# Kernel optimization log

Measured on AMD Instinct MI355X. Metric: run time of the kernel, lower is better.

## Reference

```python
import jax, jax.numpy as jnp
import numpy as np

P_CLAMP = 10.0      # opt.p
OUTPUT_SCALE = 0.1  # opt.output_scale
S_LR = 0.1          # s_lr passed to step()
R_DIM, C_DIM, HID, NLAYERS = 8192, 2048, 20, 2


def _lstm_one_step(x, h0, c0, layers):
    # x: (B, 1) single-time-step input; h0, c0: (NLAYERS, B, HID)
    # torch gate order: i, f, g, o
    inp = x
    for l, (Wih, Whh, bih, bhh) in enumerate(layers):
        gates = inp @ Wih.T + bih + h0[l] @ Whh.T + bhh  # (B, 4H)
        i, f, g, o = jnp.split(gates, 4, axis=-1)
        c = jax.nn.sigmoid(f) * c0[l] + jax.nn.sigmoid(i) * jnp.tanh(g)
        inp = jax.nn.sigmoid(o) * jnp.tanh(c)
    return inp  # last-layer hidden state (B, HID)


def _orth_proj(M, G):
    # tangent projection on the Stiefel manifold
    A = M.T @ G                      # (c, c)
    A_sym = 0.5 * (A + A.T)
    return G - M @ A_sym


def _retraction(M, P):
    Q, R = jnp.linalg.qr(M + P)      # reduced QR, M+P is (r, c), r >= c
    sign = jnp.sign(jnp.sign(jnp.diagonal(R)) + 0.5)  # maps 0 -> +1
    return Q * sign[None, :]


def _log_sign_diag(gram_diag):
    # diagonal of LogAndSign_Preprocess_Gradient: clamp(log|x|/p, -1, 1)
    return jnp.clip(jnp.log(jnp.abs(gram_diag)) / P_CLAMP, -1.0, 1.0)[:, None]


def reference(s, s_grad, L_h0, L_c0, R_h0, R_c0, L_before, R_before,
              W_ih0, W_hh0, b_ih0, b_hh0, W_ih1, W_hh1, b_ih1, b_hh1,
              L_W, L_b, R_W, R_b):
    s0 = s.shape[0]
    M = s.reshape(s0, -1).T                   # (r, c)
    M_grad = s_grad.reshape(s0, -1).T * S_LR  # (r, c)
    r, c = M.shape
    G = _orth_proj(M, M_grad)
    # only the diagonals of GG^T/c and G^TG/r are ever used by the preprocess
    ggt_diag = jnp.sum(G * G, axis=1) / c     # (r,)
    gtg_diag = jnp.sum(G * G, axis=0) / r     # (c,)
    layers = [(W_ih0, W_hh0, b_ih0, b_hh0), (W_ih1, W_hh1, b_ih1, b_hh1)]
    hl = _lstm_one_step(_log_sign_diag(ggt_diag), L_h0, L_c0, layers)  # (r, H)
    hr = _lstm_one_step(_log_sign_diag(gtg_diag), R_h0, R_c0, layers)  # (c, H)
    l_ = (hl @ L_W.T + L_b).squeeze(-1) * OUTPUT_SCALE
    l_ = l_ - l_.mean() + 1.0
    r_ = (hr @ R_W.T + R_b).squeeze(-1) * OUTPUT_SCALE
    r_ = r_ - r_.mean() + 1.0
    Lv = jnp.maximum(l_, L_before)            # diag matrices stored as vectors
    Rv = jnp.maximum(r_, R_before)
    P = Lv[:, None] * G * Rv[None, :]         # L @ G @ R with diagonal L, R
    P = _orth_proj(M, P)
    new_s = _retraction(M, -P).T.reshape(s.shape)
    return new_s


def setup_inputs() -> dict:
    key = jax.random.key(0)
    ks = jax.random.split(key, 16)
    H4 = 4 * HID
    return {
        "s": jax.random.normal(ks[0], (C_DIM, R_DIM), jnp.float32) * 0.02,
        "s_grad": jax.random.normal(ks[1], (C_DIM, R_DIM), jnp.float32) * 0.02,
        "L_h0": jax.random.normal(ks[2], (NLAYERS, R_DIM, HID), jnp.float32) * 0.1,
        "L_c0": jax.random.normal(ks[3], (NLAYERS, R_DIM, HID), jnp.float32) * 0.1,
        "R_h0": jax.random.normal(ks[4], (NLAYERS, C_DIM, HID), jnp.float32) * 0.1,
        "R_c0": jax.random.normal(ks[5], (NLAYERS, C_DIM, HID), jnp.float32) * 0.1,
        "L_before": jnp.ones((R_DIM,), jnp.float32),
        "R_before": jnp.ones((C_DIM,), jnp.float32),
        "W_ih0": jax.random.normal(ks[6], (H4, 1), jnp.float32) * 0.2,
        "W_hh0": jax.random.normal(ks[7], (H4, HID), jnp.float32) * 0.2,
        "b_ih0": jax.random.normal(ks[8], (H4,), jnp.float32) * 0.1,
        "b_hh0": jax.random.normal(ks[9], (H4,), jnp.float32) * 0.1,
        "W_ih1": jax.random.normal(ks[10], (H4, HID), jnp.float32) * 0.2,
        "W_hh1": jax.random.normal(ks[11], (H4, HID), jnp.float32) * 0.2,
        "b_ih1": jax.random.normal(ks[12], (H4,), jnp.float32) * 0.1,
        "b_hh1": jax.random.normal(ks[13], (H4,), jnp.float32) * 0.1,
        "L_W": jax.random.normal(ks[14], (1, HID), jnp.float32) * 0.2,
        "L_b": jnp.zeros((1,), jnp.float32),
        "R_W": jax.random.normal(ks[15], (1, HID), jnp.float32) * 0.2,
        "R_b": jnp.zeros((1,), jnp.float32),
    }
```

## Files before the change

kernel.cpp:

```cpp
#include <hip/hip_runtime.h>
#include <math.h>

#define RD 8192
#define CD 2048

typedef _Float16 f16x8 __attribute__((ext_vector_type(8)));
typedef _Float16 f16x4 __attribute__((ext_vector_type(4)));
typedef float    f32x4 __attribute__((ext_vector_type(4)));

#define GLOBAL_AS __attribute__((address_space(1)))
#define LDS_AS    __attribute__((address_space(3)))

__global__ __launch_bounds__(256) void gemm_nt_f16(
    const _Float16* __restrict__ A, const _Float16* __restrict__ B,
    float* __restrict__ Cp, _Float16* __restrict__ Of16,
    const float* __restrict__ Dg, const _Float16* __restrict__ Eg,
    int M, int N, int K, int ksplit, float beta, float gamma, float sgn)
{
  __shared__ __align__(1024) _Float16 As[2][128 * 32];
  __shared__ __align__(1024) _Float16 Bs[2][128 * 32];
  const int tid = threadIdx.x;
  const int wave = tid >> 6, lane = tid & 63;
  const int wy = wave >> 1, wx = wave & 1;
  const int bi = blockIdx.y * 128, bj = blockIdx.x * 128;
  const int kchunk = K / ksplit;
  const long k0 = (long)blockIdx.z * kchunk;

  f32x4 acc[4][4];
#pragma unroll
  for (int i = 0; i < 4; ++i)
#pragma unroll
    for (int j = 0; j < 4; ++j) acc[i][j] = (f32x4){0.f, 0.f, 0.f, 0.f};

  const int srow = wave * 16 + (lane >> 2);
  const int skof = (lane & 3) * 8;
  const _Float16* aA = A + (long)(bi + srow) * K + k0 + skof;
  const _Float16* aB = B + (long)(bj + srow) * K + k0 + skof;
  const int ldso = wave * 16 * 32;

#define STAGE(buf, kt)                                                         \
  {                                                                            \
    _Float16* lA = &As[buf][ldso];                                             \
    _Float16* lB = &Bs[buf][ldso];                                             \
    _Pragma("unroll")                                                          \
    for (int q = 0; q < 2; ++q) {                                              \
      __builtin_amdgcn_global_load_lds(                                        \
          (const GLOBAL_AS unsigned int*)(aA + (long)q * 64 * K + (kt)),       \
          (LDS_AS unsigned int*)(lA + q * 64 * 32), 16, 0, 0);                 \
      __builtin_amdgcn_global_load_lds(                                        \
          (const GLOBAL_AS unsigned int*)(aB + (long)q * 64 * K + (kt)),       \
          (LDS_AS unsigned int*)(lB + q * 64 * 32), 16, 0, 0);                 \
    }                                                                          \
  }

  const int fr = lane & 15;
  const int fk = (lane >> 4) * 8;

  STAGE(0, 0);
  __syncthreads();
  int cur = 0;
  for (int kt = 0; kt < kchunk; kt += 32) {
    if (kt + 32 < kchunk) STAGE(cur ^ 1, kt + 32);

    f16x8 af[4], bf[4];
#pragma unroll
    for (int t = 0; t < 4; ++t) {
      af[t] = *(const f16x8*)(&As[cur][(wy * 64 + t * 16 + fr) * 32 + fk]);
      bf[t] = *(const f16x8*)(&Bs[cur][(wx * 64 + t * 16 + fr) * 32 + fk]);
    }
#pragma unroll
    for (int mt = 0; mt < 4; ++mt)
#pragma unroll
      for (int nt = 0; nt < 4; ++nt)
        acc[mt][nt] = __builtin_amdgcn_mfma_f32_16x16x32_f16(af[mt], bf[nt], acc[mt][nt], 0, 0, 0);

    __syncthreads();
    cur ^= 1;
  }
#undef STAGE

  const int quad = lane >> 4, fc = lane & 15;
  if (Cp) {
#pragma unroll
    for (int mt = 0; mt < 4; ++mt)
#pragma unroll
      for (int nt = 0; nt < 4; ++nt) {
        const int col = bj + wx * 64 + nt * 16 + fc;
#pragma unroll
        for (int reg = 0; reg < 4; ++reg) {
          const int row = bi + wy * 64 + mt * 16 + quad * 4 + reg;
          atomicAdd(&Cp[(long)row * N + col], acc[mt][nt][reg]);
        }
      }
  } else {
#pragma unroll
    for (int mt = 0; mt < 4; ++mt)
#pragma unroll
      for (int nt = 0; nt < 4; ++nt) {
        const int col = bj + wx * 64 + nt * 16 + fc;
#pragma unroll
        for (int reg = 0; reg < 4; ++reg) {
          const int row = bi + wy * 64 + mt * 16 + quad * 4 + reg;
          const long off = (long)row * N + col;
          float v = sgn * acc[mt][nt][reg];
          if (Dg) v += beta * Dg[off];
          if (Eg) v += gamma * (float)Eg[off];
          Of16[off] = (_Float16)v;
        }
      }
  }
}

__global__ __launch_bounds__(256) void sym_combine(
    const float* __restrict__ Cp, float* __restrict__ out, int n, int nsplit, float scale)
{
  __shared__ float Ts[64][68];
  const int tid = threadIdx.x;
  const int tx = tid & 15, ty = tid >> 4;
  const int bi = blockIdx.y * 64, bj = blockIdx.x * 64;
  float acc[4][4];
#pragma unroll
  for (int i = 0; i < 4; ++i)
#pragma unroll
    for (int j = 0; j < 4; ++j) acc[i][j] = 0.f;

  for (int s = 0; s < nsplit; ++s) {
    const float* C = Cp + (long)s * n * n;
#pragma unroll
    for (int i = 0; i < 4; ++i) {
      float4 v = *(const float4*)(C + (long)(bi + ty * 4 + i) * n + bj + tx * 4);
      acc[i][0] += v.x; acc[i][1] += v.y; acc[i][2] += v.z; acc[i][3] += v.w;
    }
    __syncthreads();
#pragma unroll
    for (int i = 0; i < 4; ++i) {
      float4 w = *(const float4*)(C + (long)(bj + ty * 4 + i) * n + bi + tx * 4);
      *(float4*)&Ts[ty * 4 + i][tx * 4] = w;
    }
    __syncthreads();
#pragma unroll
    for (int i = 0; i < 4; ++i)
#pragma unroll
      for (int j = 0; j < 4; ++j) acc[i][j] += Ts[tx * 4 + j][ty * 4 + i];
  }
#pragma unroll
  for (int i = 0; i < 4; ++i) {
    float4 v; v.x = scale * acc[i][0]; v.y = scale * acc[i][1]; v.z = scale * acc[i][2]; v.w = scale * acc[i][3];
    *(float4*)(out + (long)(bi + ty * 4 + i) * n + bj + tx * 4) = v;
  }
}

__global__ __launch_bounds__(256) void cast_f16(const float* __restrict__ s, _Float16* __restrict__ d)
{
  const long i = ((long)blockIdx.x * 256 + threadIdx.x) * 4;
  float4 v = *(const float4*)(s + i);
  f16x4 o; o[0] = (_Float16)v.x; o[1] = (_Float16)v.y; o[2] = (_Float16)v.z; o[3] = (_Float16)v.w;
  *(f16x4*)(d + i) = o;
}

__global__ __launch_bounds__(256) void cast_f32(const _Float16* __restrict__ s, float* __restrict__ d)
{
  const long i = ((long)blockIdx.x * 256 + threadIdx.x) * 8;
  f16x8 v = *(const f16x8*)(s + i);
  float4 a, b;
  a.x = (float)v[0]; a.y = (float)v[1]; a.z = (float)v[2]; a.w = (float)v[3];
  b.x = (float)v[4]; b.y = (float)v[5]; b.z = (float)v[6]; b.w = (float)v[7];
  *(float4*)(d + i) = a;
  *(float4*)(d + i + 4) = b;
}

__global__ __launch_bounds__(256) void transpose_cast_f16(
    const float* __restrict__ src, _Float16* __restrict__ dst)
{
  __shared__ float T[64][65];
  const int tid = threadIdx.x, tx = tid & 15, ty = tid >> 4;
  const int r0 = blockIdx.x * 64, c0 = blockIdx.y * 64;
#pragma unroll
  for (int i = 0; i < 4; ++i) {
    float4 v = *(const float4*)(src + (long)(c0 + ty * 4 + i) * RD + r0 + tx * 4);
    T[ty * 4 + i][tx * 4 + 0] = v.x; T[ty * 4 + i][tx * 4 + 1] = v.y;
    T[ty * 4 + i][tx * 4 + 2] = v.z; T[ty * 4 + i][tx * 4 + 3] = v.w;
  }
  __syncthreads();
#pragma unroll
  for (int i = 0; i < 4; ++i) {
    f16x4 o;
#pragma unroll
    for (int j = 0; j < 4; ++j) o[j] = (_Float16)T[tx * 4 + j][ty * 4 + i];
    *(f16x4*)(dst + (long)(r0 + ty * 4 + i) * CD + c0 + tx * 4) = o;
  }
}

__global__ __launch_bounds__(256) void transpose_f16(
    const _Float16* __restrict__ src, _Float16* __restrict__ dst)
{
  __shared__ _Float16 T[64][72];
  const int tid = threadIdx.x;
  const int r0 = blockIdx.y * 64;
  const int c0 = blockIdx.x * 64;
  const int sr = tid >> 2, sc = (tid & 3) * 16;
  {
    f16x8 a = *(const f16x8*)(src + (long)(r0 + sr) * RD + c0 + sc);
    f16x8 b = *(const f16x8*)(src + (long)(r0 + sr) * RD + c0 + sc + 8);
    *(f16x8*)&T[sr][sc] = a;
    *(f16x8*)&T[sr][sc + 8] = b;
  }
  __syncthreads();
  {
    f16x8 a, b;
#pragma unroll
    for (int q = 0; q < 8; ++q) { a[q] = T[sc + q][sr]; b[q] = T[sc + 8 + q][sr]; }
    *(f16x8*)(dst + (long)(c0 + sr) * CD + r0 + sc) = a;
    *(f16x8*)(dst + (long)(c0 + sr) * CD + r0 + sc + 8) = b;
  }
}

__global__ __launch_bounds__(256) void row_sumsq(const _Float16* __restrict__ G, float* __restrict__ out, float inv)
{
  __shared__ float red[256];
  const int tid = threadIdx.x;
  const _Float16* row = G + (long)blockIdx.x * RD;
  float s = 0.f;
  for (int c = tid * 8; c < RD; c += 2048) {
    f16x8 v = *(const f16x8*)(row + c);
#pragma unroll
    for (int u = 0; u < 8; ++u) { float f = (float)v[u]; s += f * f; }
  }
  red[tid] = s; __syncthreads();
  for (int off = 128; off > 0; off >>= 1) { if (tid < off) red[tid] += red[tid + off]; __syncthreads(); }
  if (tid == 0) out[blockIdx.x] = red[0] * inv;
}

__global__ __launch_bounds__(256) void col_sumsq(const _Float16* __restrict__ G, float* __restrict__ out)
{
  const int rr = blockIdx.x * 256 + threadIdx.x;
  const int cc0 = blockIdx.y * 256;
  float s = 0.f;
  for (int i = 0; i < 256; ++i) {
    float v = (float)G[(long)(cc0 + i) * RD + rr];
    s += v * v;
  }
  atomicAdd(&out[rr], s * (1.f / (float)CD));
}

__device__ __forceinline__ float sigm_(float x) { return 1.f / (1.f + __expf(-x)); }
__device__ __forceinline__ float tanh_(float x) { float e = __expf(2.f * x); return 1.f - 2.f / (e + 1.f); }

__global__ __launch_bounds__(256) void lstm_head(
    const float* __restrict__ diag, int B,
    const float* __restrict__ h0, const float* __restrict__ c0,
    const float* __restrict__ Wih0, const float* __restrict__ Whh0,
    const float* __restrict__ bih0, const float* __restrict__ bhh0,
    const float* __restrict__ Wih1, const float* __restrict__ Whh1,
    const float* __restrict__ bih1, const float* __restrict__ bhh1,
    const float* __restrict__ HW, const float* __restrict__ Hb,
    float* __restrict__ pre, float* __restrict__ sum_out)
{
  __shared__ float w0[80], wh0[1600], b0[80], wi1[1600], wh1[1600], b1[80], hw[20];
  __shared__ float red[256];
  const int tid = threadIdx.x;
  for (int i = tid; i < 80; i += 256) { w0[i] = Wih0[i]; b0[i] = bih0[i] + bhh0[i]; b1[i] = bih1[i] + bhh1[i]; }
  for (int i = tid; i < 1600; i += 256) { wh0[i] = Whh0[i]; wi1[i] = Wih1[i]; wh1[i] = Whh1[i]; }
  if (tid < 20) hw[tid] = HW[tid];
  __syncthreads();

  const int b = blockIdx.x * 256 + tid;
  const float d = diag[b];
  float x = logf(fabsf(d)) * 0.1f;
  x = fminf(fmaxf(x, -1.f), 1.f);

  const float* h0p = h0 + (long)b * 20;
  const float* c0p = c0 + (long)b * 20;
  const float* h1p = h0 + (long)B * 20 + (long)b * 20;
  const float* c1p = c0 + (long)B * 20 + (long)b * 20;

  float h0r[20], hA[20];
#pragma unroll
  for (int m = 0; m < 20; ++m) h0r[m] = h0p[m];
#pragma unroll
  for (int h = 0; h < 20; ++h) {
    float gi = w0[h] * x + b0[h];
    float gf = w0[20 + h] * x + b0[20 + h];
    float gg = w0[40 + h] * x + b0[40 + h];
    float go = w0[60 + h] * x + b0[60 + h];
#pragma unroll
    for (int m = 0; m < 20; ++m) {
      const float hm = h0r[m];
      gi += wh0[h * 20 + m] * hm;
      gf += wh0[(20 + h) * 20 + m] * hm;
      gg += wh0[(40 + h) * 20 + m] * hm;
      go += wh0[(60 + h) * 20 + m] * hm;
    }
    const float cc = sigm_(gf) * c0p[h] + sigm_(gi) * tanh_(gg);
    hA[h] = sigm_(go) * tanh_(cc);
  }
  float h1r[20];
#pragma unroll
  for (int m = 0; m < 20; ++m) h1r[m] = h1p[m];
  float pr = 0.f;
#pragma unroll
  for (int h = 0; h < 20; ++h) {
    float gi = b1[h], gf = b1[20 + h], gg = b1[40 + h], go = b1[60 + h];
#pragma unroll
    for (int m = 0; m < 20; ++m) {
      const float am = hA[m], hm = h1r[m];
      gi += wi1[h * 20 + m] * am + wh1[h * 20 + m] * hm;
      gf += wi1[(20 + h) * 20 + m] * am + wh1[(20 + h) * 20 + m] * hm;
      gg += wi1[(40 + h) * 20 + m] * am + wh1[(40 + h) * 20 + m] * hm;
      go += wi1[(60 + h) * 20 + m] * am + wh1[(60 + h) * 20 + m] * hm;
    }
    const float cc = sigm_(gf) * c1p[h] + sigm_(gi) * tanh_(gg);
    pr += sigm_(go) * tanh_(cc) * hw[h];
  }
  pr = (pr + Hb[0]) * 0.1f;
  pre[b] = pr;

  red[tid] = pr; __syncthreads();
  for (int off = 128; off > 0; off >>= 1) { if (tid < off) red[tid] += red[tid + off]; __syncthreads(); }
  if (tid == 0) atomicAdd(sum_out, red[0]);
}

__global__ __launch_bounds__(256) void scale_P(
    _Float16* __restrict__ G, const float* __restrict__ lpre, const float* __restrict__ rpre,
    const float* __restrict__ Lbef, const float* __restrict__ Rbef, const float* __restrict__ sums)
{
  const long id4 = ((long)blockIdx.x * 256 + threadIdx.x) * 4;
  const int cc = (int)(id4 >> 13);
  const int rr = (int)(id4 & (RD - 1));
  const float meanl = sums[0] * (1.f / (float)RD);
  const float meanr = sums[1] * (1.f / (float)CD);
  const float rv = fmaxf(rpre[cc] - meanr + 1.f, Rbef[cc]);
  f16x4 g = *(f16x4*)(G + id4);
  float4 lp = *(const float4*)(lpre + rr);
  float4 lb = *(const float4*)(Lbef + rr);
  g[0] = (_Float16)((float)g[0] * rv * fmaxf(lp.x - meanl + 1.f, lb.x));
  g[1] = (_Float16)((float)g[1] * rv * fmaxf(lp.y - meanl + 1.f, lb.y));
  g[2] = (_Float16)((float)g[2] * rv * fmaxf(lp.z - meanl + 1.f, lb.z));
  g[3] = (_Float16)((float)g[3] * rv * fmaxf(lp.w - meanl + 1.f, lb.w));
  *(f16x4*)(G + id4) = g;
}

__device__ __forceinline__ void potrf_block_dev(
    float* __restrict__ S, float* __restrict__ W, float* __restrict__ KinvA,
    int d, int kprev, float (*Ls)[68], float (*Ws)[68], float (*Ts)[68])
{
  const int tid = threadIdx.x;
  const int tx = tid & 15, ty = tid >> 4;
  const long dofs = (long)d * 64;

  for (int t = tid; t < 4096; t += 256) {
    int r = t >> 6, c = t & 63;
    Ls[r][c] = S[(dofs + r) * CD + dofs + c];
  }

  if (kprev >= 0) {
    const float* Kp = KinvA + (long)kprev * 4096;
    const long ko = (long)kprev * 64;
    for (int t = tid; t < 4096; t += 256) {
      int r = t >> 6, c = t & 63;
      Ts[r][c] = S[(dofs + r) * CD + ko + c];
      Ws[r][c] = Kp[t];
    }
    __syncthreads();
    float u[4][4];
#pragma unroll
    for (int i = 0; i < 4; ++i)
#pragma unroll
      for (int j = 0; j < 4; ++j) u[i][j] = 0.f;
    for (int m = 0; m < 64; ++m) {
      float a[4], k2[4];
#pragma unroll
      for (int q = 0; q < 4; ++q) { a[q] = Ts[ty * 4 + q][m]; k2[q] = Ws[m][tx * 4 + q]; }
#pragma unroll
      for (int i = 0; i < 4; ++i)
#pragma unroll
        for (int j = 0; j < 4; ++j) u[i][j] += a[i] * k2[j];
    }
    __syncthreads();
#pragma unroll
    for (int i = 0; i < 4; ++i)
#pragma unroll
      for (int j = 0; j < 4; ++j) Ws[ty * 4 + i][tx * 4 + j] = u[i][j];
    __syncthreads();
    float acc[4][4];
#pragma unroll
    for (int i = 0; i < 4; ++i)
#pragma unroll
      for (int j = 0; j < 4; ++j) acc[i][j] = 0.f;
    for (int m = 0; m < 64; ++m) {
      float a[4], b2[4];
#pragma unroll
      for (int q = 0; q < 4; ++q) { a[q] = Ws[ty * 4 + q][m]; b2[q] = Ts[tx * 4 + q][m]; }
#pragma unroll
      for (int i = 0; i < 4; ++i)
#pragma unroll
        for (int j = 0; j < 4; ++j) acc[i][j] += a[i] * b2[j];
    }
#pragma unroll
    for (int i = 0; i < 4; ++i)
#pragma unroll
      for (int j = 0; j < 4; ++j) Ls[ty * 4 + i][tx * 4 + j] -= acc[i][j];
  }

  for (int j = 0; j < 64; ++j) {
    __syncthreads();
    const float invd = 1.f / Ls[j][j];
    for (int i = j + 1 + ty; i < 64; i += 16) {
      const float vi = Ls[i][j] * invd;
      for (int c = j + 1 + tx; c <= i; c += 16)
        Ls[i][c] -= vi * Ls[c][j];
    }
  }
  __syncthreads();
  if (tid < 64) Ts[0][tid] = 1.f / sqrtf(Ls[tid][tid]);
  __syncthreads();
  for (int t = tid; t < 4096; t += 256) {
    int r = t >> 6, c = t & 63;
    if (c <= r) Ls[r][c] *= Ts[0][c];
  }
  for (int t = tid; t < 4096; t += 256) { int r = t >> 6, c = t & 63; Ws[r][c] = 0.f; }
  __syncthreads();

  {
    const int w = tid >> 6, l = tid & 63;
    if (l < 16) {
      const int o = w * 16, c = l;
      float wr[16];
#pragma unroll
      for (int m = 0; m < 16; ++m) {
        float s = 0.f;
#pragma unroll
        for (int k = 0; k < m; ++k) s += Ls[o + m][o + k] * wr[k];
        const float rli = 1.f / Ls[o + m][o + m];
        wr[m] = (m == c) ? rli : -s * rli;
      }
#pragma unroll
      for (int m = 0; m < 16; ++m) Ws[o + m][o + c] = (m < c) ? 0.f : wr[m];
    }
  }
  __syncthreads();

  {
    for (int e = tid; e < 512; e += 256) {
      const int p = e >> 8, m = (e >> 4) & 15, c = e & 15, b0 = p * 32;
      float s = 0.f;
#pragma unroll
      for (int k = 0; k < 16; ++k) s += Ls[b0 + 16 + m][b0 + k] * Ws[b0 + k][b0 + c];
      Ts[p * 16 + m][c] = s;
    }
    __syncthreads();
    for (int e = tid; e < 512; e += 256) {
      const int p = e >> 8, m = (e >> 4) & 15, c = e & 15, b0 = p * 32;
      float s = 0.f;
#pragma unroll
      for (int k = 0; k < 16; ++k) s += Ws[b0 + 16 + m][b0 + 16 + k] * Ts[p * 16 + k][c];
      Ws[b0 + 16 + m][b0 + c] = -s;
    }
  }
  __syncthreads();

  {
    for (int q = 0; q < 4; ++q) {
      const int e = tid + 256 * q, m = e >> 5, c = e & 31;
      float s = 0.f;
#pragma unroll
      for (int k = 0; k < 32; ++k) s += Ls[32 + m][k] * Ws[k][c];
      Ts[m][c] = s;
    }
    __syncthreads();
    for (int q = 0; q < 4; ++q) {
      const int e = tid + 256 * q, m = e >> 5, c = e & 31;
      float s = 0.f;
#pragma unroll
      for (int k = 0; k < 32; ++k) s += Ws[32 + m][32 + k] * Ts[k][c];
      Ws[32 + m][c] = -s;
    }
  }
  __syncthreads();

  for (int t = tid; t < 4096; t += 256) {
    int r = t >> 6, c = t & 63;
    W[(dofs + r) * 2048 + dofs + c] = Ws[r][c];
  }
  {
    float acc[4][4];
#pragma unroll
    for (int i = 0; i < 4; ++i)
#pragma unroll
      for (int j = 0; j < 4; ++j) acc[i][j] = 0.f;
    for (int m = 0; m < 64; ++m) {
      float a[4], b2[4];
#pragma unroll
      for (int q = 0; q < 4; ++q) { a[q] = Ws[m][ty * 4 + q]; b2[q] = Ws[m][tx * 4 + q]; }
#pragma unroll
      for (int i = 0; i < 4; ++i)
#pragma unroll
        for (int j = 0; j < 4; ++j) acc[i][j] += a[i] * b2[j];
    }
    float* Kd = KinvA + (long)d * 4096;
#pragma unroll
    for (int i = 0; i < 4; ++i)
#pragma unroll
      for (int j = 0; j < 4; ++j)
        Kd[(ty * 4 + i) * 64 + tx * 4 + j] = acc[i][j];
  }
}

__global__ __launch_bounds__(256) void potrf_seed(
    float* __restrict__ S, float* __restrict__ W, float* __restrict__ KinvA)
{
  __shared__ float Ls[64][68];
  __shared__ float Ws[64][68];
  __shared__ float Ts[64][68];
  potrf_block_dev(S, W, KinvA, 0, -1, Ls, Ws, Ts);
}

__global__ __launch_bounds__(256) void ptstep_f(
    float* __restrict__ S, float* __restrict__ W, float* __restrict__ KinvA, int kb)
{
  __shared__ float As[64][68];
  __shared__ float Bs[64][68];
  __shared__ float Ts[64][68];
  const int tid = threadIdx.x, tx = tid & 15, ty = tid >> 4;
  const long ko = (long)kb * 64;
  const int nrem = 31 - kb;

  if (blockIdx.y == (unsigned)(nrem + 1)) {
    if (blockIdx.x != 0) return;
    potrf_block_dev(S, W, KinvA, kb + 1, kb, As, Bs, Ts);
    return;
  }

  if (blockIdx.y == 0) {
    const int ib = kb + 1 + blockIdx.x;
    const long ro = (long)ib * 64;
    for (int t = tid; t < 4096; t += 256) {
      int r = t >> 6, c = t & 63;
      As[r][c] = S[(ro + r) * CD + ko + c];
      Bs[r][c] = W[(ko + r) * 2048 + ko + c];
    }
    __syncthreads();
    float acc[4][4];
#pragma unroll
    for (int i = 0; i < 4; ++i)
#pragma unroll
      for (int j = 0; j < 4; ++j) acc[i][j] = 0.f;
    for (int m = 0; m < 64; ++m) {
      float a[4], w[4];
#pragma unroll
      for (int q = 0; q < 4; ++q) { a[q] = As[ty * 4 + q][m]; w[q] = Bs[tx * 4 + q][m]; }
#pragma unroll
      for (int i = 0; i < 4; ++i)
#pragma unroll
        for (int j = 0; j < 4; ++j) acc[i][j] += a[i] * w[j];
    }
#pragma unroll
    for (int i = 0; i < 4; ++i)
#pragma unroll
      for (int j = 0; j < 4; ++j)
        S[(ko + tx * 4 + j) * CD + ro + ty * 4 + i] = acc[i][j];
  } else {
    const int ib = kb + blockIdx.y;
    const int jb = kb + 1 + blockIdx.x;
    if (jb > ib) return;
    if (blockIdx.y == 1 && blockIdx.x == 0) return;
    const long io = (long)ib * 64, jo = (long)jb * 64;
    const float* Kp = KinvA + (long)kb * 4096;
    for (int t = tid; t < 4096; t += 256) {
      int r = t >> 6, c = t & 63;
      As[r][c] = S[(io + r) * CD + ko + c];
      Bs[r][c] = Kp[t];
    }
    __syncthreads();
    float acc[4][4];
#pragma unroll
    for (int i = 0; i < 4; ++i)
#pragma unroll
      for (int j = 0; j < 4; ++j) acc[i][j] = 0.f;
    for (int m = 0; m < 64; ++m) {
      float a[4], k2[4];
#pragma unroll
      for (int q = 0; q < 4; ++q) { a[q] = As[ty * 4 + q][m]; k2[q] = Bs[m][tx * 4 + q]; }
#pragma unroll
      for (int i = 0; i < 4; ++i)
#pragma unroll
        for (int j = 0; j < 4; ++j) acc[i][j] += a[i] * k2[j];
    }
#pragma unroll
    for (int i = 0; i < 4; ++i)
#pragma unroll
      for (int j = 0; j < 4; ++j) Ts[ty * 4 + i][tx * 4 + j] = acc[i][j];
    __syncthreads();
    for (int t = tid; t < 4096; t += 256) {
      int r = t >> 6, c = t & 63;
      Bs[r][c] = S[(jo + r) * CD + ko + c];
    }
    __syncthreads();
    float acc2[4][4];
#pragma unroll
    for (int i = 0; i < 4; ++i)
#pragma unroll
      for (int j = 0; j < 4; ++j) acc2[i][j] = 0.f;
    for (int m = 0; m < 64; ++m) {
      float t2[4], b2[4];
#pragma unroll
      for (int q = 0; q < 4; ++q) { t2[q] = Ts[ty * 4 + q][m]; b2[q] = Bs[tx * 4 + q][m]; }
#pragma unroll
      for (int i = 0; i < 4; ++i)
#pragma unroll
        for (int j = 0; j < 4; ++j) acc2[i][j] += t2[i] * b2[j];
    }
#pragma unroll
    for (int i = 0; i < 4; ++i)
#pragma unroll
      for (int j = 0; j < 4; ++j)
        S[(io + ty * 4 + i) * CD + jo + tx * 4 + j] -= acc2[i][j];
  }
}

__global__ __launch_bounds__(256) void winv_tn(
    const float* __restrict__ S, const float* __restrict__ W, float* __restrict__ T, int s)
{
  __shared__ float Ua[16][68];
  __shared__ float Wa[16][68];
  const int tid = threadIdx.x, tx = tid & 15, ty = tid >> 4;
  const int p = blockIdx.z, b = 2 * p * s;
  const int i0 = blockIdx.y * 64, j0 = blockIdx.x * 64;
  const int sr = tid >> 4, sc = (tid & 15) * 4;
  float acc[4][4];
#pragma unroll
  for (int i = 0; i < 4; ++i)
#pragma unroll
    for (int j = 0; j < 4; ++j) acc[i][j] = 0.f;

  for (int k0 = 0; k0 < s; k0 += 16) {
    __syncthreads();
    {
      float4 u = *(const float4*)(S + (long)(b + k0 + sr) * CD + (b + s) + i0 + sc);
      *(float4*)&Ua[sr][sc] = u;
      float4 w = *(const float4*)(W + (long)(b + k0 + sr) * 2048 + b + j0 + sc);
      *(float4*)&Wa[sr][sc] = w;
    }
    __syncthreads();
#pragma unroll
    for (int kk = 0; kk < 16; ++kk) {
      float a[4], w2[4];
#pragma unroll
      for (int q = 0; q < 4; ++q) { a[q] = Ua[kk][ty * 4 + q]; w2[q] = Wa[kk][tx * 4 + q]; }
#pragma unroll
      for (int i = 0; i < 4; ++i)
#pragma unroll
        for (int j = 0; j < 4; ++j) acc[i][j] += a[i] * w2[j];
    }
  }
  float* Tp = T + (long)p * s * s;
#pragma unroll
  for (int i = 0; i < 4; ++i)
#pragma unroll
    for (int j = 0; j < 4; ++j)
      Tp[(long)(i0 + ty * 4 + i) * s + j0 + tx * 4 + j] = acc[i][j];
}

__global__ __launch_bounds__(256) void winv_nn(
    float* __restrict__ W, const float* __restrict__ T, int s)
{
  __shared__ float Wc[64][20];
  __shared__ float Tt[16][68];
  const int tid = threadIdx.x, tx = tid & 15, ty = tid >> 4;
  const int p = blockIdx.z, b = 2 * p * s, bs = b + s;
  const int i0 = blockIdx.y * 64, j0 = blockIdx.x * 64;
  const float* Tp = T + (long)p * s * s;
  float acc[4][4];
#pragma unroll
  for (int i = 0; i < 4; ++i)
#pragma unroll
    for (int j = 0; j < 4; ++j) acc[i][j] = 0.f;

  for (int k0 = 0; k0 < s; k0 += 16) {
    __syncthreads();
    {
      const int wr = tid >> 2, wc = (tid & 3) * 4;
      float4 a = *(const float4*)(W + (long)(bs + i0 + wr) * 2048 + bs + k0 + wc);
      *(float4*)&Wc[wr][wc] = a;
      const int tr = tid >> 4, tc = (tid & 15) * 4;
      float4 t2 = *(const float4*)(Tp + (long)(k0 + tr) * s + j0 + tc);
      *(float4*)&Tt[tr][tc] = t2;
    }
    __syncthreads();
#pragma unroll
    for (int kk = 0; kk < 16; ++kk) {
      float a[4], t3[4];
#pragma unroll
      for (int q = 0; q < 4; ++q) { a[q] = Wc[ty * 4 + q][kk]; t3[q] = Tt[kk][tx * 4 + q]; }
#pragma unroll
      for (int i = 0; i < 4; ++i)
#pragma unroll
        for (int j = 0; j < 4; ++j) acc[i][j] += a[i] * t3[j];
    }
  }
#pragma unroll
  for (int i = 0; i < 4; ++i)
#pragma unroll
    for (int j = 0; j < 4; ++j)
      W[(long)(bs + i0 + ty * 4 + i) * 2048 + b + j0 + tx * 4 + j] = -acc[i][j];
}

extern "C" void kernel_launch(void* const* d_in, const int* in_sizes, int n_in,
                              void* d_out, int out_size, void* d_ws, size_t ws_size,
                              hipStream_t stream)
{
  const float* s_in  = (const float*)d_in[0];
  const float* sgrad = (const float*)d_in[1];
  const float* L_h0  = (const float*)d_in[2];
  const float* L_c0  = (const float*)d_in[3];
  const float* R_h0  = (const float*)d_in[4];
  const float* R_c0  = (const float*)d_in[5];
  const float* L_bef = (const float*)d_in[6];
  const float* R_bef = (const float*)d_in[7];
  const float* Wih0  = (const float*)d_in[8];
  const float* Whh0  = (const float*)d_in[9];
  const float* bih0  = (const float*)d_in[10];
  const float* bhh0  = (const float*)d_in[11];
  const float* Wih1  = (const float*)d_in[12];
  const float* Whh1  = (const float*)d_in[13];
  const float* bih1  = (const float*)d_in[14];
  const float* bhh1  = (const float*)d_in[15];
  const float* L_W   = (const float*)d_in[16];
  const float* L_b   = (const float*)d_in[17];
  const float* R_W   = (const float*)d_in[18];
  const float* R_b   = (const float*)d_in[19];

  float* out = (float*)d_out;
  char*  ws  = (char*)d_ws;

  const size_t SYM_OFF = (size_t)1 << 17;
  const size_t OVL_OFF = SYM_OFF + ((size_t)16 << 20);
  const size_t BIG_OFF = OVL_OFF + ((size_t)32 << 20);
  float* vec  = (float*)ws;
  float* sums = vec;
  float* ggt  = vec + 4;
  float* gtg  = ggt + RD;
  float* lpre = gtg + CD;
  float* rpre = lpre + RD;
  float*     SYM  = (float*)(ws + SYM_OFF);
  float*     Cp   = (float*)(ws + OVL_OFF);
  _Float16*  SYMh = (_Float16*)(ws + OVL_OFF);
  float*     Wf   = (float*)(ws + OVL_OFF + ((size_t)1 << 20));
  _Float16*  Wh   = (_Float16*)(ws + OVL_OFF + ((size_t)17 << 20));
  float*     Tbuf = (float*)(ws + OVL_OFF + ((size_t)25 << 20));
  float*     KinvA= (float*)(ws + OVL_OFF + ((size_t)29 << 20));
  _Float16*  BIG  = (_Float16*)(ws + BIG_OFF);

  _Float16* Mt_h  = (_Float16*)d_out;
  _Float16* slotB = Mt_h + (long)CD * RD;
  _Float16* Xtr   = (_Float16*)d_out;

  hipMemsetAsync(vec, 0, (4 + RD) * sizeof(float), stream);
  hipMemsetAsync(Cp, 0, (size_t)CD * CD * sizeof(float), stream);

  const dim3 blk(256);
  const dim3 gK8(16, 16, 8);
  const dim3 gK2(64, 16, 1);
  const dim3 gSym(32, 32);
  const int  castBlocks = (CD * RD / 4) / 256;

  cast_f16<<<castBlocks, blk, 0, stream>>>(s_in, Mt_h);
  cast_f16<<<castBlocks, blk, 0, stream>>>(sgrad, slotB);

  gemm_nt_f16<<<gK8, blk, 0, stream>>>(Mt_h, slotB, Cp, nullptr, nullptr, nullptr,
                                       CD, CD, RD, 8, 0.f, 0.f, 1.f);
  sym_combine<<<gSym, blk, 0, stream>>>(Cp, SYM, CD, 1, 0.05f);
  cast_f16<<<(CD * CD / 4) / 256, blk, 0, stream>>>(SYM, SYMh);

  transpose_cast_f16<<<dim3(RD / 64, CD / 64), blk, 0, stream>>>(s_in, slotB);

  gemm_nt_f16<<<gK2, blk, 0, stream>>>(SYMh, slotB, nullptr, BIG, sgrad, nullptr,
                                       CD, RD, CD, 1, 0.1f, 0.f, -1.f);

  row_sumsq<<<CD, blk, 0, stream>>>(BIG, gtg, 1.f / (float)RD);
  col_sumsq<<<dim3(RD / 256, CD / 256), blk, 0, stream>>>(BIG, ggt);

  lstm_head<<<RD / 256, blk, 0, stream>>>(ggt, RD, L_h0, L_c0, Wih0, Whh0, bih0, bhh0,
                                          Wih1, Whh1, bih1, bhh1, L_W, L_b, lpre, &sums[0]);
  lstm_head<<<CD / 256, blk, 0, stream>>>(gtg, CD, R_h0, R_c0, Wih0, Whh0, bih0, bhh0,
                                          Wih1, Whh1, bih1, bhh1, R_W, R_b, rpre, &sums[1]);

  scale_P<<<(CD * (RD / 4)) / 256, blk, 0, stream>>>(BIG, lpre, rpre, L_bef, R_bef, sums);

  hipMemsetAsync(Cp, 0, (size_t)CD * CD * sizeof(float), stream);
  gemm_nt_f16<<<gK8, blk, 0, stream>>>(Mt_h, BIG, Cp, nullptr, nullptr, nullptr,
                                       CD, CD, RD, 8, 0.f, 0.f, 1.f);
  sym_combine<<<gSym, blk, 0, stream>>>(Cp, SYM, CD, 1, 0.5f);
  cast_f16<<<(CD * CD / 4) / 256, blk, 0, stream>>>(SYM, SYMh);

  gemm_nt_f16<<<gK2, blk, 0, stream>>>(SYMh, slotB, nullptr, BIG, s_in, BIG,
                                       CD, RD, CD, 1, 1.f, -1.f, 1.f);

  hipMemsetAsync(Cp, 0, (size_t)CD * CD * sizeof(float), stream);
  gemm_nt_f16<<<gK8, blk, 0, stream>>>(BIG, BIG, Cp, nullptr, nullptr, nullptr,
                                       CD, CD, RD, 8, 0.f, 0.f, 1.f);
  sym_combine<<<gSym, blk, 0, stream>>>(Cp, SYM, CD, 1, 0.5f);

  hipMemsetAsync(Wf, 0, (size_t)CD * CD * sizeof(float), stream);
  transpose_f16<<<dim3(RD / 64, CD / 64), blk, 0, stream>>>(BIG, Xtr);

  potrf_seed<<<1, blk, 0, stream>>>(SYM, Wf, KinvA);
  for (int kb = 0; kb < 31; ++kb) {
    const int nrem = 31 - kb;
    ptstep_f<<<dim3(nrem, nrem + 2), blk, 0, stream>>>(SYM, Wf, KinvA, kb);
  }

  for (int lev = 0; lev < 5; ++lev) {
    const int s = 64 << lev, npairs = 16 >> lev;
    const dim3 g(s / 64, s / 64, npairs);
    winv_tn<<<g, blk, 0, stream>>>(SYM, Wf, Tbuf, s);
    winv_nn<<<g, blk, 0, stream>>>(Wf, Tbuf, s);
  }

  cast_f16<<<(CD * CD / 4) / 256, blk, 0, stream>>>(Wf, Wh);
  gemm_nt_f16<<<gK2, blk, 0, stream>>>(Wh, Xtr, nullptr, BIG, nullptr, nullptr,
                                       CD, RD, CD, 1, 0.f, 0.f, 1.f);
  cast_f32<<<(CD * RD / 8) / 256, blk, 0, stream>>>(BIG, out);
}
```

Measured before the change: 3.171 ms.

## Deepen GEMM LDS pipeline to four stages with explicit vmcnt waits

Replaces the double-buffered LDS pipeline in the f16 MFMA GEMM with a four-slot ring that keeps two tiles in flight ahead of compute. Each iteration waits only on the older loads using partial s_waitcnt vmcnt counts plus a raw barrier, instead of a full __syncthreads after every tile. The goal is to hide more global-load latency behind MFMA work. In exchange, LDS use doubles to 64KB per block, which may lower occupancy, and the code assumes kchunk covers at least two tiles.

```diff
diff --git a/kernel.cpp b/kernel.cpp
--- a/kernel.cpp
+++ b/kernel.cpp
@@ -17,8 +17,8 @@
     const float* __restrict__ Dg, const _Float16* __restrict__ Eg,
     int M, int N, int K, int ksplit, float beta, float gamma, float sgn)
 {
-  __shared__ __align__(1024) _Float16 As[2][128 * 32];
-  __shared__ __align__(1024) _Float16 Bs[2][128 * 32];
+  __shared__ __align__(1024) _Float16 As[4][128 * 32];
+  __shared__ __align__(1024) _Float16 Bs[4][128 * 32];
   const int tid = threadIdx.x;
   const int wave = tid >> 6, lane = tid & 63;
   const int wy = wave >> 1, wx = wave & 1;
@@ -56,28 +56,39 @@
   const int fr = lane & 15;
   const int fk = (lane >> 4) * 8;
 
+#define COMPUTE(slot)                                                          \
+  {                                                                            \
+    f16x8 af[4], bf[4];                                                        \
+    _Pragma("unroll")                                                          \
+    for (int t = 0; t < 4; ++t) {                                              \
+      af[t] = *(const f16x8*)(&As[slot][(wy * 64 + t * 16 + fr) * 32 + fk]);   \
+      bf[t] = *(const f16x8*)(&Bs[slot][(wx * 64 + t * 16 + fr) * 32 + fk]);   \
+    }                                                                          \
+    _Pragma("unroll")                                                          \
+    for (int mt = 0; mt < 4; ++mt)                                             \
+      _Pragma("unroll")                                                        \
+      for (int nt = 0; nt < 4; ++nt)                                           \
+        acc[mt][nt] = __builtin_amdgcn_mfma_f32_16x16x32_f16(                  \
+            af[mt], bf[nt], acc[mt][nt], 0, 0, 0);                             \
+  }
+
+  const int nt_ = kchunk >> 5;
   STAGE(0, 0);
-  __syncthreads();
-  int cur = 0;
-  for (int kt = 0; kt < kchunk; kt += 32) {
-    if (kt + 32 < kchunk) STAGE(cur ^ 1, kt + 32);
-
-    f16x8 af[4], bf[4];
-#pragma unroll
-    for (int t = 0; t < 4; ++t) {
-      af[t] = *(const f16x8*)(&As[cur][(wy * 64 + t * 16 + fr) * 32 + fk]);
-      bf[t] = *(const f16x8*)(&Bs[cur][(wx * 64 + t * 16 + fr) * 32 + fk]);
-    }
-#pragma unroll
-    for (int mt = 0; mt < 4; ++mt)
-#pragma unroll
-      for (int nt = 0; nt < 4; ++nt)
-        acc[mt][nt] = __builtin_amdgcn_mfma_f32_16x16x32_f16(af[mt], bf[nt], acc[mt][nt], 0, 0, 0);
-
-    __syncthreads();
-    cur ^= 1;
-  }
+  STAGE(1, 32);
+  for (int i = 0; i + 2 < nt_; ++i) {
+    STAGE((i + 2) & 3, (i + 2) * 32);
+    asm volatile("s_waitcnt vmcnt(8)" ::: "memory");
+    __builtin_amdgcn_s_barrier();
+    COMPUTE(i & 3);
+  }
+  asm volatile("s_waitcnt vmcnt(4)" ::: "memory");
+  __builtin_amdgcn_s_barrier();
+  COMPUTE((nt_ - 2) & 3);
+  asm volatile("s_waitcnt vmcnt(0)" ::: "memory");
+  __builtin_amdgcn_s_barrier();
+  COMPUTE((nt_ - 1) & 3);
 #undef STAGE
+#undef COMPUTE
 
   const int quad = lane >> 4, fc = lane & 15;
   if (Cp) {
```

After: 3.217 ms. About the same (+1.4%).
